# Performance work log

Measured on AMD Instinct MI355X. Metric: run time of the kernel, lower is better.

## Reference

```python
import jax, jax.numpy as jnp
import numpy as np

B, C, S = 256, 3, 224  # [batch, line, s, s] per RRN's data.size() usage


def setup_inputs() -> dict:
    key = jax.random.key(0)
    k_x, k_lap, k_bern = jax.random.split(key, 3)
    eps = 1  # privacy budget; p = e^eps / (1 + e^eps) = sigmoid(eps)
    p = jax.nn.sigmoid(jnp.float32(eps))
    x = jax.random.uniform(k_x, (B, C, S, S), dtype=jnp.float32)
    # Laplace(0,1) noise, same for every batch element as drawn independently
    laplace_noise = jax.random.laplace(k_lap, (B, C, S, S), dtype=jnp.float32)
    # np.random.choice([0,1], p=[p, 1-p]) -> 1 with prob (1-p)
    mask = (jax.random.uniform(k_bern, (B, C, S, S), dtype=jnp.float32) >= p).astype(jnp.float32)
    return {"x": x, "eps": eps, "laplace_noise": laplace_noise, "mask": mask}


def reference(x, eps, laplace_noise, mask):
    # RRN: data[i] = clamp(data[i] + laplace * bernoulli_mask, 0, 1), vectorized over batch.
    # eps only parameterizes the Bernoulli keep-probability, already baked into `mask`.
    return jnp.clip(x + laplace_noise * mask, 0.0, 1.0)
```

## Files before the change

### kernel.cpp

```cpp
#include <hip/hip_runtime.h>


__global__ __launch_bounds__(256) void rrn_clip_kernel(
    const float4* __restrict__ x,
    const float4* __restrict__ lap,
    const float4* __restrict__ mask,
    float4* __restrict__ out,
    int n4)
{
    int i = blockIdx.x * blockDim.x + threadIdx.x;
    if (i >= n4) return;

    float4 xv = x[i];
    float4 lv = lap[i];
    float4 mv = mask[i];

    float4 o;
    o.x = fminf(fmaxf(fmaf(lv.x, mv.x, xv.x), 0.0f), 1.0f);
    o.y = fminf(fmaxf(fmaf(lv.y, mv.y, xv.y), 0.0f), 1.0f);
    o.z = fminf(fmaxf(fmaf(lv.z, mv.z, xv.z), 0.0f), 1.0f);
    o.w = fminf(fmaxf(fmaf(lv.w, mv.w, xv.w), 0.0f), 1.0f);

    out[i] = o;
}

extern "C" void kernel_launch(void* const* d_in, const int* in_sizes, int n_in,
                              void* d_out, int out_size, void* d_ws, size_t ws_size,
                              hipStream_t stream)
{
    const float4* x    = (const float4*)d_in[0];
    const float4* lap  = (const float4*)d_in[2];
    const float4* mask = (const float4*)d_in[3];
    float4* out        = (float4*)d_out;

    int n  = out_size;
    int n4 = n >> 2;

    const int block = 256;
    const int grid  = (n4 + block - 1) / block;

    rrn_clip_kernel<<<grid, block, 0, stream>>>(x, lap, mask, out, n4);
}
```

Before: 433.5 us.

## Use grid-stride loop with 4x unrolled loads and nontemporal stores

Replaces the one-thread-per-float4 launch with a fixed 2048-block grid-stride loop. Each iteration issues twelve independent vector loads before computing, which raises memory-level parallelism per thread. Outputs are written with nontemporal stores so the streaming write does not pollute cache. The risk is that a fixed grid may underfill or imbalance the GPU compared with the fully sized launch.

```diff
diff --git a/kernel.cpp b/kernel.cpp
--- a/kernel.cpp
+++ b/kernel.cpp
@@ -1,43 +1,70 @@
 #include <hip/hip_runtime.h>
 
 
+typedef float fvec4 __attribute__((ext_vector_type(4)));
+
+__device__ __forceinline__ fvec4 clip_fma(fvec4 l, fvec4 m, fvec4 xv) {
+    fvec4 o;
+    o.x = fminf(fmaxf(fmaf(l.x, m.x, xv.x), 0.0f), 1.0f);
+    o.y = fminf(fmaxf(fmaf(l.y, m.y, xv.y), 0.0f), 1.0f);
+    o.z = fminf(fmaxf(fmaf(l.z, m.z, xv.z), 0.0f), 1.0f);
+    o.w = fminf(fmaxf(fmaf(l.w, m.w, xv.w), 0.0f), 1.0f);
+    return o;
+}
+
 __global__ __launch_bounds__(256) void rrn_clip_kernel(
-    const float4* __restrict__ x,
-    const float4* __restrict__ lap,
-    const float4* __restrict__ mask,
-    float4* __restrict__ out,
+    const fvec4* __restrict__ x,
+    const fvec4* __restrict__ lap,
+    const fvec4* __restrict__ mask,
+    fvec4* __restrict__ out,
     int n4)
 {
-    int i = blockIdx.x * blockDim.x + threadIdx.x;
-    if (i >= n4) return;
+    const int tid    = blockIdx.x * blockDim.x + threadIdx.x;
+    const int stride = gridDim.x * blockDim.x;
 
-    float4 xv = x[i];
-    float4 lv = lap[i];
-    float4 mv = mask[i];
+    int i = tid;
 
-    float4 o;
-    o.x = fminf(fmaxf(fmaf(lv.x, mv.x, xv.x), 0.0f), 1.0f);
-    o.y = fminf(fmaxf(fmaf(lv.y, mv.y, xv.y), 0.0f), 1.0f);
-    o.z = fminf(fmaxf(fmaf(lv.z, mv.z, xv.z), 0.0f), 1.0f);
-    o.w = fminf(fmaxf(fmaf(lv.w, mv.w, xv.w), 0.0f), 1.0f);
+    for (; i + 3 * stride < n4; i += 4 * stride) {
+        const int i0 = i;
+        const int i1 = i + stride;
+        const int i2 = i + 2 * stride;
+        const int i3 = i + 3 * stride;
 
-    out[i] = o;
+        fvec4 x0 = x[i0],    x1 = x[i1],    x2 = x[i2],    x3 = x[i3];
+        fvec4 l0 = lap[i0],  l1 = lap[i1],  l2 = lap[i2],  l3 = lap[i3];
+        fvec4 m0 = mask[i0], m1 = mask[i1], m2 = mask[i2], m3 = mask[i3];
+
+        fvec4 o0 = clip_fma(l0, m0, x0);
+        fvec4 o1 = clip_fma(l1, m1, x1);
+        fvec4 o2 = clip_fma(l2, m2, x2);
+        fvec4 o3 = clip_fma(l3, m3, x3);
+
+        __builtin_nontemporal_store(o0, &out[i0]);
+        __builtin_nontemporal_store(o1, &out[i1]);
+        __builtin_nontemporal_store(o2, &out[i2]);
+        __builtin_nontemporal_store(o3, &out[i3]);
+    }
+
+    for (; i < n4; i += stride) {
+        fvec4 o = clip_fma(lap[i], mask[i], x[i]);
+        __builtin_nontemporal_store(o, &out[i]);
+    }
 }
 
 extern "C" void kernel_launch(void* const* d_in, const int* in_sizes, int n_in,
                               void* d_out, int out_size, void* d_ws, size_t ws_size,
                               hipStream_t stream)
 {
-    const float4* x    = (const float4*)d_in[0];
-    const float4* lap  = (const float4*)d_in[2];
-    const float4* mask = (const float4*)d_in[3];
-    float4* out        = (float4*)d_out;
+    const fvec4* x    = (const fvec4*)d_in[0];
+    const fvec4* lap  = (const fvec4*)d_in[2];
+    const fvec4* mask = (const fvec4*)d_in[3];
+    fvec4* out        = (fvec4*)d_out;
 
-    int n  = out_size;
-    int n4 = n >> 2;
+    const int n  = out_size;
+    const int n4 = n >> 2;
 
     const int block = 256;
-    const int grid  = (n4 + block - 1) / block;
+    const int grid  = 2048;
 
     rrn_clip_kernel<<<grid, block, 0, stream>>>(x, lap, mask, out, n4);
 }
```

New measurement: 462.2 us. 6.6% more time.
